# Optimization experiments

Hardware: AMD Instinct MI355X
Metric: run time of the kernel (lower is better)

Reference implementation:

```python
import jax, jax.numpy as jnp
import numpy as np

B, N, D, H, S = 64, 1000, 512, 8, 20
DK = D // H
TANH_CLIP = 10.0
NEG = -1e9


def setup_inputs() -> dict:
    key = jax.random.key(0)
    k1, k2, k3, k4, k5 = jax.random.split(key, 5)
    embeddings = jax.random.normal(k1, (B, N, D), dtype=jnp.float32)
    q = jax.random.normal(k2, (B, S, D), dtype=jnp.float32)
    # action_mask: True = feasible. Ensure at least one feasible node per row.
    action_mask = jax.random.bernoulli(k3, 0.5, (B, S, N))
    action_mask = action_mask.at[:, :, 0].set(True)
    W_kvl = jax.random.normal(k4, (D, 3 * D), dtype=jnp.float32) * (1.0 / np.sqrt(D))
    W_out = jax.random.normal(k5, (D, D), dtype=jnp.float32) * (1.0 / np.sqrt(D))
    return {"embeddings": embeddings, "q": q, "action_mask": action_mask,
            "W_kvl": W_kvl, "W_out": W_out}


def reference(embeddings, q, action_mask, W_kvl, W_out):
    # _precompute: project node embeddings into glimpse K, V and logit K
    kvl = jnp.einsum('bnd,de->bne', embeddings, W_kvl)  # [B,N,3D]
    glimpse_k, glimpse_v, logit_k = jnp.split(kvl, 3, axis=-1)
    # dynamic embedding is zero (StaticEmbedding for TSP)

    mask = ~action_mask  # True = infeasible, shape [B,S,N]

    # multi-head glimpse attention
    qh = q.reshape(B, S, H, DK)
    kh = glimpse_k.reshape(B, N, H, DK)
    vh = glimpse_v.reshape(B, N, H, DK)
    compat = jnp.einsum('bshd,bnhd->bhsn', qh, kh) / np.sqrt(DK)
    compat = jnp.where(mask[:, None, :, :], NEG, compat)
    attn = jax.nn.softmax(compat, axis=-1)
    heads = jnp.einsum('bhsn,bnhd->bshd', attn, vh).reshape(B, S, D)
    glimpse = jnp.einsum('bsd,de->bse', heads, W_out)  # [B,S,D]

    # pointer logits against logit_k, tanh clipping, mask, log-softmax
    logits = jnp.einsum('bsd,bnd->bsn', glimpse, logit_k) / np.sqrt(D)
    logits = TANH_CLIP * jnp.tanh(logits)
    logits = jnp.where(mask, NEG, logits)
    log_p = jax.nn.log_softmax(logits, axis=-1)  # [B,S,N]

    # rearrange 'b s l -> (s b) l'
    return jnp.swapaxes(log_p, 0, 1).reshape(S * B, N)
```

## Files before the change

### kernel.cpp

```cpp
#include <hip/hip_runtime.h>

#define BB 64
#define NN 1000
#define NP 1024
#define DD 512
#define HH 8
#define SS 20
#define NEGV -1e9f

typedef float v4f __attribute__((ext_vector_type(4)));
typedef short v8s __attribute__((ext_vector_type(8)));
typedef int   v8i __attribute__((ext_vector_type(8)));
typedef int   v4i __attribute__((ext_vector_type(4)));
typedef unsigned char uchar;
typedef unsigned long long ulong_t;

static __device__ __forceinline__ short f2bf(float f) {
    unsigned u = __builtin_bit_cast(unsigned, f);
    u = (u + 0x7fffu + ((u >> 16) & 1u)) >> 16;
    return (short)u;
}
static __device__ __forceinline__ float bf2f(short s) {
    unsigned u = ((unsigned)(unsigned short)s) << 16;
    return __builtin_bit_cast(float, u);
}
static __device__ __forceinline__ uchar f2fp8(float f) {
    return (uchar)(__builtin_amdgcn_cvt_pk_fp8_f32(f, 0.f, 0, false) & 0xff);
}

static __device__ __forceinline__ void gld16(const void* g, void* l) {
    __builtin_amdgcn_global_load_lds(
        (const __attribute__((address_space(1))) void*)(g),
        (__attribute__((address_space(3))) void*)(l),
        16, 0, 0);
}

__global__ void prep(const float* __restrict__ Wkvl, uchar* __restrict__ Wt8,
                     const float* __restrict__ Wout, short* __restrict__ Wot,
                     const float* __restrict__ emb, int* __restrict__ emb8) {
    __shared__ float t[32][33];
    int bid = blockIdx.x, tid = threadIdx.x;
    if (bid < 768) {
        int c0 = (bid % 48) * 32, r0 = (bid / 48) * 32;
        int x = tid & 31, y = tid >> 5;
        for (int k = 0; k < 32; k += 8)
            t[y + k][x] = Wkvl[(long)(r0 + y + k) * 1536 + c0 + x];
        __syncthreads();
        for (int k = 0; k < 32; k += 8)
            Wt8[(long)(c0 + y + k) * 512 + r0 + x] = f2fp8(t[x][y + k]);
    } else if (bid < 1024) {
        int bb = bid - 768;
        int c0 = (bb & 15) * 32, r0 = (bb >> 4) * 32;
        int x = tid & 31, y = tid >> 5;
        for (int k = 0; k < 32; k += 8)
            t[y + k][x] = Wout[(long)(r0 + y + k) * 512 + c0 + x];
        __syncthreads();
        for (int k = 0; k < 32; k += 8)
            Wot[(long)(c0 + y + k) * 512 + r0 + x] = f2bf(t[x][y + k]);
    } else {
        int i = (bid - 1024) * 256 + tid;
        long o = (long)i * 8;
        v4f a = *(const v4f*)(emb + o);
        v4f b = *(const v4f*)(emb + o + 4);
        int lo = __builtin_amdgcn_cvt_pk_fp8_f32(a.x, a.y, 0, false);
        lo = __builtin_amdgcn_cvt_pk_fp8_f32(a.z, a.w, lo, true);
        int hi = __builtin_amdgcn_cvt_pk_fp8_f32(b.x, b.y, 0, false);
        hi = __builtin_amdgcn_cvt_pk_fp8_f32(b.z, b.w, hi, true);
        int2 r; r.x = lo; r.y = hi;
        *(int2*)(emb8 + i * 2) = r;
    }
}

__global__ __launch_bounds__(256) void gemm_kvl(const uchar* __restrict__ emb8,
                                                const uchar* __restrict__ Wt8,
                                                uchar* __restrict__ kvl8) {
    extern __shared__ __align__(16) uchar smem[];
    uchar* As0 = smem;
    uchar* Bs0 = smem + 32768;
    int tid = threadIdx.x;
    int id = blockIdx.x;
    int wgid = (id & 7) * 750 + (id >> 3);
    int m_idx = wgid / 12, n_idx = wgid - m_idx * 12;
    int m0 = m_idx * 128, n0 = n_idx * 128;
    int wid = tid >> 6, lane = tid & 63, quad = lane >> 4, l16 = lane & 15;
    int wm = wid & 1, wn = wid >> 1;
    const uchar* Ag = emb8 + (long)m0 * 512;
    const uchar* Bg = Wt8 + (long)n0 * 512;
    int rsub = lane >> 3;
    int kc = ((lane & 7) ^ rsub) * 16;

    v4f acc[4][4] = {};

    auto stageAB = [&](int bi, int kk) {
        #pragma unroll
        for (int p = 0; p < 4; ++p) {
            int rl = wid * 32 + p * 8;
            gld16(Ag + (long)(rl + rsub) * 512 + kk + kc, As0 + bi * 16384 + rl * 128);
        }
        #pragma unroll
        for (int p = 0; p < 4; ++p) {
            int rl = wid * 32 + p * 8;
            gld16(Bg + (long)(rl + rsub) * 512 + kk + kc, Bs0 + bi * 16384 + rl * 128);
        }
    };
    auto ldfrag = [&](const uchar* base, int row) -> v8i {
        int c0 = (quad * 2) ^ (row & 7);
        v4i lo = *(const v4i*)(base + row * 128 + c0 * 16);
        v4i hi = *(const v4i*)(base + row * 128 + (c0 ^ 1) * 16);
        return __builtin_shufflevector(lo, hi, 0, 1, 2, 3, 4, 5, 6, 7);
    };

    stageAB(0, 0);
    stageAB(1, 128);
    asm volatile("s_waitcnt vmcnt(8)" ::: "memory");
    __builtin_amdgcn_s_barrier();
    __builtin_amdgcn_sched_barrier(0);

    v8i af[4], bf[4];
    #pragma unroll
    for (int t = 0; t < 4; ++t) {
        int cur = t & 1;
        const uchar* ab = As0 + cur * 16384;
        const uchar* bb = Bs0 + cur * 16384;
        #pragma unroll
        for (int i = 0; i < 4; ++i) af[i] = ldfrag(ab, wm * 64 + i * 16 + l16);
        #pragma unroll
        for (int j = 0; j < 4; ++j) bf[j] = ldfrag(bb, wn * 64 + j * 16 + l16);
        __builtin_amdgcn_s_setprio(1);
        #pragma unroll
        for (int i = 0; i < 4; ++i)
            #pragma unroll
            for (int j = 0; j < 2; ++j)
                acc[i][j] = __builtin_amdgcn_mfma_scale_f32_16x16x128_f8f6f4(
                    af[i], bf[j], acc[i][j], 0, 0, 0, 0x7f7f7f7f, 0, 0x7f7f7f7f);
        __builtin_amdgcn_s_setprio(0);
        asm volatile("s_waitcnt lgkmcnt(0)" ::: "memory");
        __builtin_amdgcn_s_barrier();
        if (t < 2) stageAB(cur, (t + 2) * 128);
        __builtin_amdgcn_s_setprio(1);
        #pragma unroll
        for (int i = 0; i < 4; ++i)
            #pragma unroll
            for (int j = 2; j < 4; ++j)
                acc[i][j] = __builtin_amdgcn_mfma_scale_f32_16x16x128_f8f6f4(
                    af[i], bf[j], acc[i][j], 0, 0, 0, 0x7f7f7f7f, 0, 0x7f7f7f7f);
        __builtin_amdgcn_s_setprio(0);
        if (t < 3) {
            if (t < 2) asm volatile("s_waitcnt vmcnt(8)" ::: "memory");
            else       asm volatile("s_waitcnt vmcnt(0)" ::: "memory");
            __builtin_amdgcn_s_barrier();
            __builtin_amdgcn_sched_barrier(0);
        }
    }
    __syncthreads();

    short* rp = (short*)smem;
    short* r = rp + wid * (16 * 72);
    #pragma unroll
    for (int i = 0; i < 4; ++i) {
        #pragma unroll
        for (int jj = 0; jj < 4; ++jj)
            #pragma unroll
            for (int rr = 0; rr < 4; ++rr)
                r[(quad * 4 + rr) * 72 + jj * 16 + l16] = f2bf(acc[i][jj][rr]);
        #pragma unroll
        for (int h = 0; h < 2; ++h) {
            int rowl = h * 8 + (lane >> 3);
            int colc = (lane & 7) * 8;
            v8s val = *(const v8s*)(r + rowl * 72 + colc);
            int lo = __builtin_amdgcn_cvt_pk_fp8_f32(bf2f(val[0]), bf2f(val[1]), 0, false);
            lo = __builtin_amdgcn_cvt_pk_fp8_f32(bf2f(val[2]), bf2f(val[3]), lo, true);
            int hi = __builtin_amdgcn_cvt_pk_fp8_f32(bf2f(val[4]), bf2f(val[5]), 0, false);
            hi = __builtin_amdgcn_cvt_pk_fp8_f32(bf2f(val[6]), bf2f(val[7]), hi, true);
            int2 st; st.x = lo; st.y = hi;
            *(int2*)(kvl8 + (long)(m0 + wm * 64 + i * 16 + rowl) * 1536 +
                     n0 + wn * 64 + colc) = st;
        }
    }
}

__global__ void pack_kv(const uchar* __restrict__ kvl8, uchar* __restrict__ Kf,
                        uchar* __restrict__ Vf) {
    int bh = blockIdx.x, b = bh >> 3, h = bh & 7;
    int g = blockIdx.y;
    __shared__ uchar Kl[64][72];
    __shared__ uchar VT[64][72];
    int tid = threadIdx.x;
    int node_l = tid >> 2, chunk = (tid & 3) * 16;
    int gn = g * 64 + node_l;
    int ncl = gn < NN ? gn : NN - 1;
    const uchar* rowp = kvl8 + ((long)b * NN + ncl) * 1536 + h * 64;
    *(v4i*)&Kl[node_l][chunk] = *(const v4i*)(rowp + chunk);
    {
        const uchar* vp = rowp + 512 + chunk;
        ulong_t v0 = *(const ulong_t*)(vp);
        ulong_t v1 = *(const ulong_t*)(vp + 8);
        uchar* b0p = (uchar*)&v0; uchar* b1p = (uchar*)&v1;
        #pragma unroll
        for (int j = 0; j < 8; ++j) VT[chunk + j][node_l] = b0p[j];
        #pragma unroll
        for (int j = 0; j < 8; ++j) VT[chunk + 8 + j][node_l] = b1p[j];
    }
    __syncthreads();
    int wid = tid >> 6, lane = tid & 63, l16 = lane & 15, quad = lane >> 4;
    #pragma unroll
    for (int ks = 0; ks < 2; ++ks) {
        ulong_t frag = *(const ulong_t*)&Kl[wid * 16 + l16][ks * 32 + quad * 8];
        *(ulong_t*)(Kf + (((long)bh * 64 + g * 4 + wid) * 2 + ks) * 512 + lane * 8) = frag;
    }
    #pragma unroll
    for (int sub = 0; sub < 2; ++sub) {
        ulong_t frag = *(const ulong_t*)&VT[wid * 16 + l16][sub * 32 + quad * 8];
        *(ulong_t*)(Vf + (((long)bh * 4 + wid) * 32 + g * 2 + sub) * 512 + lane * 8) = frag;
    }
}

#define CST 1036
__global__ __launch_bounds__(512) void attn_fused(const float* __restrict__ q,
                                                  const uchar* __restrict__ Kf,
                                                  const uchar* __restrict__ Vf,
                                                  const int* __restrict__ mask,
                                                  float* __restrict__ heads) {
    int b = blockIdx.x, h = blockIdx.y;
    __shared__ __align__(16) uchar qs[32 * 72];
    __shared__ __align__(16) short cmp[SS * CST];
    int tid = threadIdx.x, wid = tid >> 6, lane = tid & 63, quad = lane >> 4, l16 = lane & 15;
    for (int i = tid; i < 32 * 64; i += 512) {
        int row = i >> 6, col = i & 63;
        float v = (row < SS) ? q[((long)b * SS + row) * DD + h * 64 + col] : 0.f;
        qs[row * 72 + col] = f2fp8(v);
    }
    __syncthreads();
    long af[2][2];
    #pragma unroll
    for (int mt = 0; mt < 2; ++mt)
        #pragma unroll
        for (int ks = 0; ks < 2; ++ks)
            af[mt][ks] = *(const long*)(qs + (mt * 16 + l16) * 72 + ks * 32 + quad * 8);
    const uchar* kfb = Kf + ((long)(b * HH + h) * 64) * 1024;
    for (int t = 0; t < 8; ++t) {
        int nt = wid * 8 + t;
        long b0 = *(const long*)(kfb + (long)nt * 1024 + lane * 8);
        long b1 = *(const long*)(kfb + (long)nt * 1024 + 512 + lane * 8);
        #pragma unroll
        for (int mt = 0; mt < 2; ++mt) {
            v4f a = {};
            a = __builtin_amdgcn_mfma_f32_16x16x32_fp8_fp8(af[mt][0], b0, a, 0, 0, 0);
            a = __builtin_amdgcn_mfma_f32_16x16x32_fp8_fp8(af[mt][1], b1, a, 0, 0, 0);
            #pragma unroll
            for (int r = 0; r < 4; ++r) {
                int s = mt * 16 + quad * 4 + r;
                if (s < SS) cmp[s * CST + nt * 16 + l16] = f2bf(a[r] * 0.125f);
            }
        }
    }
    __syncthreads();
    for (int s = wid; s < SS; s += 8) {
        const int* mr = mask + ((long)b * SS + s) * NN;
        float x[16];
        float mx = NEGV;
        #pragma unroll
        for (int i = 0; i < 16; ++i) {
            int n = lane + 64 * i;
            float v = bf2f(cmp[s * CST + n]);
            bool feas = (n < NN) && (mr[n < NN ? n : 0] != 0);
            x[i] = feas ? v : NEGV;
            mx = fmaxf(mx, x[i]);
        }
        for (int off = 32; off; off >>= 1) mx = fmaxf(mx, __shfl_xor(mx, off));
        float sum = 0.f;
        #pragma unroll
        for (int i = 0; i < 16; ++i) { x[i] = __expf(x[i] - mx); sum += x[i]; }
        for (int off = 32; off; off >>= 1) sum += __shfl_xor(sum, off);
        float inv = 1.0f / sum;
        uchar* pr = (uchar*)cmp + (long)s * (CST * 2);
        #pragma unroll
        for (int i = 0; i < 16; ++i) pr[lane + 64 * i] = f2fp8(x[i] * inv);
    }
    __syncthreads();
    int mt = wid & 1, dt = wid >> 1;
    int srow = mt * 16 + l16; if (srow > SS - 1) srow = SS - 1;
    const uchar* ap = (const uchar*)cmp + (long)srow * (CST * 2) + quad * 8;
    const uchar* vfb = Vf + (((long)(b * HH + h) * 4 + dt) * 32) * 512;
    v4f acc = {};
    for (int k0s = 0; k0s < 32; ++k0s) {
        long afr = *(const long*)(ap + k0s * 32);
        long bfr = *(const long*)(vfb + (long)k0s * 512 + lane * 8);
        acc = __builtin_amdgcn_mfma_f32_16x16x32_fp8_fp8(afr, bfr, acc, 0, 0, 0);
    }
    #pragma unroll
    for (int r = 0; r < 4; ++r) {
        int s = mt * 16 + quad * 4 + r;
        if (s < SS)
            heads[((long)b * SS + s) * DD + h * 64 + dt * 16 + l16] = acc[r];
    }
}

__global__ __launch_bounds__(256) void out_proj(const float* __restrict__ heads,
                                                const short* __restrict__ Wot,
                                                float* __restrict__ glimpse) {
    __shared__ __align__(16) short As[64 * 40], Bs[64 * 40];
    int tid = threadIdx.x;
    int m0 = blockIdx.x * 64, n0 = blockIdx.y * 64;
    int wid = tid >> 6, lane = tid & 63, quad = lane >> 4, l16 = lane & 15;
    int wm = wid & 1, wn = wid >> 1;
    int arow = tid >> 3, akol = (tid & 7) * 4;
    int brow = tid >> 2, bkol = (tid & 3) * 8;
    v4f acc[2][2] = {};
    for (int kk = 0; kk < 512; kk += 32) {
        #pragma unroll
        for (int p = 0; p < 2; ++p) {
            int r = arow + p * 32;
            v4f a = *(const v4f*)(heads + (long)(m0 + r) * 512 + kk + akol);
            short4 s4;
            s4.x = f2bf(a.x); s4.y = f2bf(a.y); s4.z = f2bf(a.z); s4.w = f2bf(a.w);
            *(short4*)(As + r * 40 + akol) = s4;
        }
        *(uint4*)(Bs + brow * 40 + bkol) =
            *(const uint4*)(Wot + (long)(n0 + brow) * 512 + kk + bkol);
        __syncthreads();
        #pragma unroll
        for (int i = 0; i < 2; ++i) {
            v8s af = *(const v8s*)(As + (wm * 32 + i * 16 + l16) * 40 + quad * 8);
            #pragma unroll
            for (int j = 0; j < 2; ++j) {
                v8s bf = *(const v8s*)(Bs + (wn * 32 + j * 16 + l16) * 40 + quad * 8);
                acc[i][j] = __builtin_amdgcn_mfma_f32_16x16x32_bf16(af, bf, acc[i][j], 0, 0, 0);
            }
        }
        __syncthreads();
    }
    #pragma unroll
    for (int i = 0; i < 2; ++i)
        #pragma unroll
        for (int j = 0; j < 2; ++j)
            #pragma unroll
            for (int r = 0; r < 4; ++r)
                glimpse[(long)(m0 + wm * 32 + i * 16 + quad * 4 + r) * 512 +
                        n0 + wn * 32 + j * 16 + l16] = acc[i][j][r];
}

__global__ __launch_bounds__(256) void ptr_logits(const float* __restrict__ glimpse,
                                                  const uchar* __restrict__ kvl8,
                                                  float* __restrict__ logits) {
    int b = blockIdx.x, g = blockIdx.y;
    __shared__ __align__(16) uchar Gs[32 * 520];
    int tid = threadIdx.x;
    #pragma unroll
    for (int it = 0; it < 16; ++it) {
        int e = it * 1024 + tid * 4;
        int row = e >> 9, col = e & 511;
        int pk = 0;
        if (row < SS) {
            v4f a = *(const v4f*)(glimpse + ((long)b * SS + row) * 512 + col);
            pk = __builtin_amdgcn_cvt_pk_fp8_f32(a.x, a.y, 0, false);
            pk = __builtin_amdgcn_cvt_pk_fp8_f32(a.z, a.w, pk, true);
        }
        *(int*)(Gs + row * 520 + col) = pk;
    }
    __syncthreads();
    int wid = tid >> 6, lane = tid & 63, quad = lane >> 4, l16 = lane & 15;
    const float scale = 0.04419417382415922f;
    int nt = g * 4 + wid;
    int n = nt * 16 + l16;
    int ncl = n < NN ? n : NN - 1;
    const uchar* kp = kvl8 + ((long)b * NN + ncl) * 1536 + 1024 + quad * 8;
    v4f acc[2] = {};
    for (int k = 0; k < 16; ++k) {
        long bfr = *(const long*)(kp + k * 32);
        #pragma unroll
        for (int m = 0; m < 2; ++m) {
            long afr = *(const long*)(Gs + (m * 16 + l16) * 520 + k * 32 + quad * 8);
            acc[m] = __builtin_amdgcn_mfma_f32_16x16x32_fp8_fp8(afr, bfr, acc[m], 0, 0, 0);
        }
    }
    #pragma unroll
    for (int m = 0; m < 2; ++m)
        #pragma unroll
        for (int r = 0; r < 4; ++r) {
            int s = m * 16 + quad * 4 + r;
            if (s < SS)
                logits[((long)b * SS + s) * NP + nt * 16 + l16] = acc[m][r] * scale;
        }
}

__global__ __launch_bounds__(256) void logsoftmax_out(const float* __restrict__ logits,
                                                      const int* __restrict__ mask,
                                                      float* __restrict__ out) {
    int row = blockIdx.x;
    int b = row / SS, s = row % SS;
    int tid = threadIdx.x;
    __shared__ float red[8];
    int n0 = tid * 4;
    v4f v = *(const v4f*)(logits + (long)row * NP + n0);
    const int* mr = mask + (long)row * NN;
    float x[4];
    float mx = NEGV;
    #pragma unroll
    for (int j = 0; j < 4; ++j) {
        int n = n0 + j;
        float t = 10.f * tanhf(v[j]);
        bool feas = (n < NN) && (mr[n < NN ? n : 0] != 0);
        x[j] = feas ? t : NEGV;
        mx = fmaxf(mx, x[j]);
    }
    for (int off = 32; off; off >>= 1) mx = fmaxf(mx, __shfl_xor(mx, off));
    int wid = tid >> 6, lane = tid & 63;
    if (lane == 0) red[wid] = mx;
    __syncthreads();
    mx = fmaxf(fmaxf(red[0], red[1]), fmaxf(red[2], red[3]));
    float sum = 0.f;
    #pragma unroll
    for (int j = 0; j < 4; ++j) sum += __expf(x[j] - mx);
    for (int off = 32; off; off >>= 1) sum += __shfl_xor(sum, off);
    __syncthreads();
    if (lane == 0) red[4 + wid] = sum;
    __syncthreads();
    sum = red[4] + red[5] + red[6] + red[7];
    float lse = mx + __logf(sum);
    float* orow = out + ((long)s * BB + b) * NN;
    #pragma unroll
    for (int j = 0; j < 4; ++j) {
        int n = n0 + j;
        if (n < NN) orow[n] = x[j] - lse;
    }
}

extern "C" void kernel_launch(void* const* d_in, const int* in_sizes, int n_in,
                              void* d_out, int out_size, void* d_ws, size_t ws_size,
                              hipStream_t stream) {
    const float* emb  = (const float*)d_in[0];
    const float* q    = (const float*)d_in[1];
    const int*   mask = (const int*)d_in[2];
    const float* Wkvl = (const float*)d_in[3];
    const float* Wout = (const float*)d_in[4];
    float* out = (float*)d_out;

    char* ws = (char*)d_ws;
    uchar* kvl8    = (uchar*)ws; ws += (size_t)64000 * 1536;
    uchar* Vt8     = (uchar*)ws; ws += (size_t)512 * 64 * NP;
    uchar* Wt8     = (uchar*)ws; ws += (size_t)1536 * 512;
    uchar* emb8    = (uchar*)ws; ws += (size_t)64000 * 512;
    short* Wot     = (short*)ws; ws += (size_t)512 * 512 * 2;
    float* heads   = (float*)ws; ws += (size_t)BB * SS * DD * 4;
    float* glimpse = (float*)ws; ws += (size_t)BB * SS * DD * 4;
    float* logits  = (float*)ws; ws += (size_t)BB * SS * NP * 4;

    uchar* Kf = Wt8;
    uchar* Vf = Vt8;

    static int s_attr_done = 0;
    if (!s_attr_done) {
        hipFuncSetAttribute(reinterpret_cast<const void*>(gemm_kvl),
                            hipFuncAttributeMaxDynamicSharedMemorySize, 65536);
        s_attr_done = 1;
    }

    prep<<<dim3(1024 + 16000), 256, 0, stream>>>(Wkvl, Wt8, Wout, Wot, emb, (int*)emb8);
    gemm_kvl<<<dim3(6000), 256, 65536, stream>>>(emb8, Wt8, kvl8);
    pack_kv<<<dim3(512, 16), 256, 0, stream>>>(kvl8, Kf, Vf);
    attn_fused<<<dim3(BB, HH), 512, 0, stream>>>(q, Kf, Vf, mask, heads);
    out_proj<<<dim3(20, 8), 256, 0, stream>>>(heads, Wot, glimpse);
    ptr_logits<<<dim3(BB, 16), 256, 0, stream>>>(glimpse, kvl8, logits);
    logsoftmax_out<<<dim3(BB * SS), 256, 0, stream>>>(logits, mask, out);
}
```

Measured before the change: 349.2 us.

## Fuse K/V fragment packing into GEMM epilogue and drop pack_kv kernel

The projection GEMM's epilogue now writes glimpse K and V straight into the MFMA-fragment layouts (Kf, and a transposed Vf) used by the attention kernel. The logit K goes to its own compact buffer with a 512-byte row stride. This removes the separate pack_kv launch and the round trip of the full 1536-wide fp8 kvl tensor through memory. The V epilogue does scattered 8-byte stores with transposition from shared memory and explicitly zeroes the padding past the last node. The attention PV loop also splits its accumulation across four independent accumulators to break the MFMA dependency chain.

```diff
diff --git a/kernel.cpp b/kernel.cpp
--- a/kernel.cpp
+++ b/kernel.cpp
@@ -73,7 +73,9 @@
 
 __global__ __launch_bounds__(256) void gemm_kvl(const uchar* __restrict__ emb8,
                                                 const uchar* __restrict__ Wt8,
-                                                uchar* __restrict__ kvl8) {
+                                                uchar* __restrict__ Kf,
+                                                uchar* __restrict__ Vf,
+                                                uchar* __restrict__ kvlL) {
     extern __shared__ __align__(16) uchar smem[];
     uchar* As0 = smem;
     uchar* Bs0 = smem + 32768;
@@ -156,6 +158,7 @@
 
     short* rp = (short*)smem;
     short* r = rp + wid * (16 * 72);
+    int nw = n0 + wn * 64;
     #pragma unroll
     for (int i = 0; i < 4; ++i) {
         #pragma unroll
@@ -163,55 +166,71 @@
             #pragma unroll
             for (int rr = 0; rr < 4; ++rr)
                 r[(quad * 4 + rr) * 72 + jj * 16 + l16] = f2bf(acc[i][jj][rr]);
-        #pragma unroll
-        for (int h = 0; h < 2; ++h) {
-            int rowl = h * 8 + (lane >> 3);
-            int colc = (lane & 7) * 8;
-            v8s val = *(const v8s*)(r + rowl * 72 + colc);
-            int lo = __builtin_amdgcn_cvt_pk_fp8_f32(bf2f(val[0]), bf2f(val[1]), 0, false);
-            lo = __builtin_amdgcn_cvt_pk_fp8_f32(bf2f(val[2]), bf2f(val[3]), lo, true);
-            int hi = __builtin_amdgcn_cvt_pk_fp8_f32(bf2f(val[4]), bf2f(val[5]), 0, false);
-            hi = __builtin_amdgcn_cvt_pk_fp8_f32(bf2f(val[6]), bf2f(val[7]), hi, true);
-            int2 st; st.x = lo; st.y = hi;
-            *(int2*)(kvl8 + (long)(m0 + wm * 64 + i * 16 + rowl) * 1536 +
-                     n0 + wn * 64 + colc) = st;
-        }
-    }
-}
-
-__global__ void pack_kv(const uchar* __restrict__ kvl8, uchar* __restrict__ Kf,
-                        uchar* __restrict__ Vf) {
-    int bh = blockIdx.x, b = bh >> 3, h = bh & 7;
-    int g = blockIdx.y;
-    __shared__ uchar Kl[64][72];
-    __shared__ uchar VT[64][72];
-    int tid = threadIdx.x;
-    int node_l = tid >> 2, chunk = (tid & 3) * 16;
-    int gn = g * 64 + node_l;
-    int ncl = gn < NN ? gn : NN - 1;
-    const uchar* rowp = kvl8 + ((long)b * NN + ncl) * 1536 + h * 64;
-    *(v4i*)&Kl[node_l][chunk] = *(const v4i*)(rowp + chunk);
-    {
-        const uchar* vp = rowp + 512 + chunk;
-        ulong_t v0 = *(const ulong_t*)(vp);
-        ulong_t v1 = *(const ulong_t*)(vp + 8);
-        uchar* b0p = (uchar*)&v0; uchar* b1p = (uchar*)&v1;
-        #pragma unroll
-        for (int j = 0; j < 8; ++j) VT[chunk + j][node_l] = b0p[j];
-        #pragma unroll
-        for (int j = 0; j < 8; ++j) VT[chunk + 8 + j][node_l] = b1p[j];
-    }
-    __syncthreads();
-    int wid = tid >> 6, lane = tid & 63, l16 = lane & 15, quad = lane >> 4;
-    #pragma unroll
-    for (int ks = 0; ks < 2; ++ks) {
-        ulong_t frag = *(const ulong_t*)&Kl[wid * 16 + l16][ks * 32 + quad * 8];
-        *(ulong_t*)(Kf + (((long)bh * 64 + g * 4 + wid) * 2 + ks) * 512 + lane * 8) = frag;
-    }
-    #pragma unroll
-    for (int sub = 0; sub < 2; ++sub) {
-        ulong_t frag = *(const ulong_t*)&VT[wid * 16 + l16][sub * 32 + quad * 8];
-        *(ulong_t*)(Vf + (((long)bh * 4 + wid) * 32 + g * 2 + sub) * 512 + lane * 8) = frag;
+        int sub0 = m0 + wm * 64 + i * 16;
+        if (n_idx < 4) {
+            int hK = nw >> 6;
+            #pragma unroll
+            for (int h2 = 0; h2 < 2; ++h2) {
+                int rowl = h2 * 8 + (lane >> 3);
+                int colc = (lane & 7) * 8;
+                v8s val = *(const v8s*)(r + rowl * 72 + colc);
+                int lo = __builtin_amdgcn_cvt_pk_fp8_f32(bf2f(val[0]), bf2f(val[1]), 0, false);
+                lo = __builtin_amdgcn_cvt_pk_fp8_f32(bf2f(val[2]), bf2f(val[3]), lo, true);
+                int hi = __builtin_amdgcn_cvt_pk_fp8_f32(bf2f(val[4]), bf2f(val[5]), 0, false);
+                hi = __builtin_amdgcn_cvt_pk_fp8_f32(bf2f(val[6]), bf2f(val[7]), hi, true);
+                int node = sub0 + rowl;
+                int b = node / 1000, nl = node - b * 1000;
+                long addr = (((long)(b * 8 + hK) * 64 + (nl >> 4)) * 2 + (colc >> 5)) * 512
+                            + ((((colc & 31) >> 3) * 16 + (nl & 15)) * 8);
+                int2 st; st.x = lo; st.y = hi;
+                *(int2*)(Kf + addr) = st;
+            }
+        } else if (n_idx < 8) {
+            int hV = (nw - 512) >> 6;
+            int o = lane >> 5, dl = lane & 31;
+            int node0 = sub0 + o * 8;
+            int b = node0 / 1000, nl = node0 - b * 1000;
+            int bh4 = (b * 8 + hV) * 4;
+            int quadv = (nl & 31) >> 3;
+            #pragma unroll
+            for (int u = 0; u < 2; ++u) {
+                int d = u * 32 + dl;
+                float f0 = bf2f(r[(o * 8 + 0) * 72 + d]);
+                float f1 = bf2f(r[(o * 8 + 1) * 72 + d]);
+                float f2 = bf2f(r[(o * 8 + 2) * 72 + d]);
+                float f3 = bf2f(r[(o * 8 + 3) * 72 + d]);
+                float f4 = bf2f(r[(o * 8 + 4) * 72 + d]);
+                float f5 = bf2f(r[(o * 8 + 5) * 72 + d]);
+                float f6 = bf2f(r[(o * 8 + 6) * 72 + d]);
+                float f7 = bf2f(r[(o * 8 + 7) * 72 + d]);
+                int lo = __builtin_amdgcn_cvt_pk_fp8_f32(f0, f1, 0, false);
+                lo = __builtin_amdgcn_cvt_pk_fp8_f32(f2, f3, lo, true);
+                int hi = __builtin_amdgcn_cvt_pk_fp8_f32(f4, f5, 0, false);
+                hi = __builtin_amdgcn_cvt_pk_fp8_f32(f6, f7, hi, true);
+                long base = ((long)(bh4 + (d >> 4)) * 32 + (nl >> 5)) * 512 + (d & 15) * 8;
+                int2 st; st.x = lo; st.y = hi;
+                *(int2*)(Vf + base + quadv * 128) = st;
+                if (nl == 992) {
+                    int2 z; z.x = 0; z.y = 0;
+                    *(int2*)(Vf + base + 1 * 128) = z;
+                    *(int2*)(Vf + base + 2 * 128) = z;
+                    *(int2*)(Vf + base + 3 * 128) = z;
+                }
+            }
+        } else {
+            #pragma unroll
+            for (int h2 = 0; h2 < 2; ++h2) {
+                int rowl = h2 * 8 + (lane >> 3);
+                int colc = (lane & 7) * 8;
+                v8s val = *(const v8s*)(r + rowl * 72 + colc);
+                int lo = __builtin_amdgcn_cvt_pk_fp8_f32(bf2f(val[0]), bf2f(val[1]), 0, false);
+                lo = __builtin_amdgcn_cvt_pk_fp8_f32(bf2f(val[2]), bf2f(val[3]), lo, true);
+                int hi = __builtin_amdgcn_cvt_pk_fp8_f32(bf2f(val[4]), bf2f(val[5]), 0, false);
+                hi = __builtin_amdgcn_cvt_pk_fp8_f32(bf2f(val[6]), bf2f(val[7]), hi, true);
+                int2 st; st.x = lo; st.y = hi;
+                *(int2*)(kvlL + (long)(sub0 + rowl) * 512 + (nw - 1024) + colc) = st;
+            }
+        }
     }
 }
 
@@ -282,17 +301,27 @@
     int srow = mt * 16 + l16; if (srow > SS - 1) srow = SS - 1;
     const uchar* ap = (const uchar*)cmp + (long)srow * (CST * 2) + quad * 8;
     const uchar* vfb = Vf + (((long)(b * HH + h) * 4 + dt) * 32) * 512;
-    v4f acc = {};
-    for (int k0s = 0; k0s < 32; ++k0s) {
-        long afr = *(const long*)(ap + k0s * 32);
-        long bfr = *(const long*)(vfb + (long)k0s * 512 + lane * 8);
-        acc = __builtin_amdgcn_mfma_f32_16x16x32_fp8_fp8(afr, bfr, acc, 0, 0, 0);
-    }
+    v4f a0 = {}, a1 = {}, a2 = {}, a3 = {};
+    for (int k0s = 0; k0s < 32; k0s += 4) {
+        a0 = __builtin_amdgcn_mfma_f32_16x16x32_fp8_fp8(
+            *(const long*)(ap + k0s * 32),
+            *(const long*)(vfb + (long)k0s * 512 + lane * 8), a0, 0, 0, 0);
+        a1 = __builtin_amdgcn_mfma_f32_16x16x32_fp8_fp8(
+            *(const long*)(ap + (k0s + 1) * 32),
+            *(const long*)(vfb + (long)(k0s + 1) * 512 + lane * 8), a1, 0, 0, 0);
+        a2 = __builtin_amdgcn_mfma_f32_16x16x32_fp8_fp8(
+            *(const long*)(ap + (k0s + 2) * 32),
+            *(const long*)(vfb + (long)(k0s + 2) * 512 + lane * 8), a2, 0, 0, 0);
+        a3 = __builtin_amdgcn_mfma_f32_16x16x32_fp8_fp8(
+            *(const long*)(ap + (k0s + 3) * 32),
+            *(const long*)(vfb + (long)(k0s + 3) * 512 + lane * 8), a3, 0, 0, 0);
+    }
+    v4f accv = (a0 + a1) + (a2 + a3);
     #pragma unroll
     for (int r = 0; r < 4; ++r) {
         int s = mt * 16 + quad * 4 + r;
         if (s < SS)
-            heads[((long)b * SS + s) * DD + h * 64 + dt * 16 + l16] = acc[r];
+            heads[((long)b * SS + s) * DD + h * 64 + dt * 16 + l16] = accv[r];
     }
 }
 
@@ -341,7 +370,7 @@
 }
 
 __global__ __launch_bounds__(256) void ptr_logits(const float* __restrict__ glimpse,
-                                                  const uchar* __restrict__ kvl8,
+                                                  const uchar* __restrict__ kvlL,
                                                   float* __restrict__ logits) {
     int b = blockIdx.x, g = blockIdx.y;
     __shared__ __align__(16) uchar Gs[32 * 520];
@@ -364,7 +393,7 @@
     int nt = g * 4 + wid;
     int n = nt * 16 + l16;
     int ncl = n < NN ? n : NN - 1;
-    const uchar* kp = kvl8 + ((long)b * NN + ncl) * 1536 + 1024 + quad * 8;
+    const uchar* kp = kvlL + ((long)b * NN + ncl) * 512 + quad * 8;
     v4f acc[2] = {};
     for (int k = 0; k < 16; ++k) {
         long bfr = *(const long*)(kp + k * 32);
@@ -437,8 +466,9 @@
     float* out = (float*)d_out;
 
     char* ws = (char*)d_ws;
-    uchar* kvl8    = (uchar*)ws; ws += (size_t)64000 * 1536;
-    uchar* Vt8     = (uchar*)ws; ws += (size_t)512 * 64 * NP;
+    uchar* kvlL    = (uchar*)ws; ws += (size_t)64000 * 512;
+    uchar* Vf      = (uchar*)ws; ws += (size_t)512 * 64 * 1024;
+    uchar* Kf      = (uchar*)ws; ws += (size_t)512 * 64 * 1024;
     uchar* Wt8     = (uchar*)ws; ws += (size_t)1536 * 512;
     uchar* emb8    = (uchar*)ws; ws += (size_t)64000 * 512;
     short* Wot     = (short*)ws; ws += (size_t)512 * 512 * 2;
@@ -446,9 +476,6 @@
     float* glimpse = (float*)ws; ws += (size_t)BB * SS * DD * 4;
     float* logits  = (float*)ws; ws += (size_t)BB * SS * NP * 4;
 
-    uchar* Kf = Wt8;
-    uchar* Vf = Vt8;
-
     static int s_attr_done = 0;
     if (!s_attr_done) {
         hipFuncSetAttribute(reinterpret_cast<const void*>(gemm_kvl),
@@ -457,10 +484,9 @@
     }
 
     prep<<<dim3(1024 + 16000), 256, 0, stream>>>(Wkvl, Wt8, Wout, Wot, emb, (int*)emb8);
-    gemm_kvl<<<dim3(6000), 256, 65536, stream>>>(emb8, Wt8, kvl8);
-    pack_kv<<<dim3(512, 16), 256, 0, stream>>>(kvl8, Kf, Vf);
+    gemm_kvl<<<dim3(6000), 256, 65536, stream>>>(emb8, Wt8, Kf, Vf, kvlL);
     attn_fused<<<dim3(BB, HH), 512, 0, stream>>>(q, Kf, Vf, mask, heads);
     out_proj<<<dim3(20, 8), 256, 0, stream>>>(heads, Wot, glimpse);
-    ptr_logits<<<dim3(BB, 16), 256, 0, stream>>>(glimpse, kvl8, logits);
+    ptr_logits<<<dim3(BB, 16), 256, 0, stream>>>(glimpse, kvlL, logits);
     logsoftmax_out<<<dim3(BB * SS), 256, 0, stream>>>(logits, mask, out);
 }
```

Measured after the change: 361.7 us. +3.6%, slower.

## Fuse output projection, pointer logits and log-softmax into one per-batch kernel

Applied to the files above, without the earlier changes.

Replaces the out_proj, ptr_logits and logsoftmax_out kernels with a single head_out kernel. It runs one 512-thread block per batch element and keeps glimpse and logits in shared memory instead of round-tripping through global memory. The attention PV loop now splits into four independent accumulators to shorten the MFMA dependency chain. The cost is that only 64 blocks run, each with about 130KB of LDS, so parallelism is much lower than the previous grids. Glimpse is also rounded to bf16 before the fp8 conversion, which adds a small extra rounding step.

```diff
diff --git a/kernel.cpp b/kernel.cpp
--- a/kernel.cpp
+++ b/kernel.cpp
@@ -282,147 +282,137 @@
     int srow = mt * 16 + l16; if (srow > SS - 1) srow = SS - 1;
     const uchar* ap = (const uchar*)cmp + (long)srow * (CST * 2) + quad * 8;
     const uchar* vfb = Vf + (((long)(b * HH + h) * 4 + dt) * 32) * 512;
-    v4f acc = {};
-    for (int k0s = 0; k0s < 32; ++k0s) {
-        long afr = *(const long*)(ap + k0s * 32);
-        long bfr = *(const long*)(vfb + (long)k0s * 512 + lane * 8);
-        acc = __builtin_amdgcn_mfma_f32_16x16x32_fp8_fp8(afr, bfr, acc, 0, 0, 0);
-    }
+    v4f a0 = {}, a1 = {}, a2 = {}, a3 = {};
+    for (int k0s = 0; k0s < 32; k0s += 4) {
+        a0 = __builtin_amdgcn_mfma_f32_16x16x32_fp8_fp8(
+            *(const long*)(ap + k0s * 32),
+            *(const long*)(vfb + (long)k0s * 512 + lane * 8), a0, 0, 0, 0);
+        a1 = __builtin_amdgcn_mfma_f32_16x16x32_fp8_fp8(
+            *(const long*)(ap + (k0s + 1) * 32),
+            *(const long*)(vfb + (long)(k0s + 1) * 512 + lane * 8), a1, 0, 0, 0);
+        a2 = __builtin_amdgcn_mfma_f32_16x16x32_fp8_fp8(
+            *(const long*)(ap + (k0s + 2) * 32),
+            *(const long*)(vfb + (long)(k0s + 2) * 512 + lane * 8), a2, 0, 0, 0);
+        a3 = __builtin_amdgcn_mfma_f32_16x16x32_fp8_fp8(
+            *(const long*)(ap + (k0s + 3) * 32),
+            *(const long*)(vfb + (long)(k0s + 3) * 512 + lane * 8), a3, 0, 0, 0);
+    }
+    v4f accv = (a0 + a1) + (a2 + a3);
     #pragma unroll
     for (int r = 0; r < 4; ++r) {
         int s = mt * 16 + quad * 4 + r;
         if (s < SS)
-            heads[((long)b * SS + s) * DD + h * 64 + dt * 16 + l16] = acc[r];
-    }
-}
-
-__global__ __launch_bounds__(256) void out_proj(const float* __restrict__ heads,
+            heads[((long)b * SS + s) * DD + h * 64 + dt * 16 + l16] = accv[r];
+    }
+}
+
+__global__ __launch_bounds__(512) void head_out(const float* __restrict__ heads,
                                                 const short* __restrict__ Wot,
-                                                float* __restrict__ glimpse) {
-    __shared__ __align__(16) short As[64 * 40], Bs[64 * 40];
-    int tid = threadIdx.x;
-    int m0 = blockIdx.x * 64, n0 = blockIdx.y * 64;
-    int wid = tid >> 6, lane = tid & 63, quad = lane >> 4, l16 = lane & 15;
-    int wm = wid & 1, wn = wid >> 1;
-    int arow = tid >> 3, akol = (tid & 7) * 4;
-    int brow = tid >> 2, bkol = (tid & 3) * 8;
-    v4f acc[2][2] = {};
+                                                const uchar* __restrict__ kvl8,
+                                                const int* __restrict__ mask,
+                                                float* __restrict__ out) {
+    extern __shared__ __align__(16) uchar hsm[];
+    short* As = (short*)hsm;
+    uchar* Gs = hsm + 33280;
+    float* Lg = (float*)(hsm + 33280 + 16640);
+    int b = blockIdx.x;
+    int tid = threadIdx.x, wid = tid >> 6, lane = tid & 63, quad = lane >> 4, l16 = lane & 15;
+
+    for (int u = tid; u < 32 * 128; u += 512) {
+        int row = u >> 7, c4 = (u & 127) * 4;
+        short4 s4;
+        if (row < SS) {
+            v4f a = *(const v4f*)(heads + ((long)b * SS + row) * 512 + c4);
+            s4.x = f2bf(a.x); s4.y = f2bf(a.y); s4.z = f2bf(a.z); s4.w = f2bf(a.w);
+        } else { s4.x = 0; s4.y = 0; s4.z = 0; s4.w = 0; }
+        *(short4*)(As + row * 520 + c4) = s4;
+    }
+    __syncthreads();
+
+    int n0w = wid * 64;
+    v4f acc[2][4] = {};
     for (int kk = 0; kk < 512; kk += 32) {
-        #pragma unroll
-        for (int p = 0; p < 2; ++p) {
-            int r = arow + p * 32;
-            v4f a = *(const v4f*)(heads + (long)(m0 + r) * 512 + kk + akol);
-            short4 s4;
-            s4.x = f2bf(a.x); s4.y = f2bf(a.y); s4.z = f2bf(a.z); s4.w = f2bf(a.w);
-            *(short4*)(As + r * 40 + akol) = s4;
-        }
-        *(uint4*)(Bs + brow * 40 + bkol) =
-            *(const uint4*)(Wot + (long)(n0 + brow) * 512 + kk + bkol);
-        __syncthreads();
-        #pragma unroll
-        for (int i = 0; i < 2; ++i) {
-            v8s af = *(const v8s*)(As + (wm * 32 + i * 16 + l16) * 40 + quad * 8);
-            #pragma unroll
-            for (int j = 0; j < 2; ++j) {
-                v8s bf = *(const v8s*)(Bs + (wn * 32 + j * 16 + l16) * 40 + quad * 8);
-                acc[i][j] = __builtin_amdgcn_mfma_f32_16x16x32_bf16(af, bf, acc[i][j], 0, 0, 0);
+        v8s afr[2], bfr[4];
+        #pragma unroll
+        for (int m = 0; m < 2; ++m)
+            afr[m] = *(const v8s*)(As + (m * 16 + l16) * 520 + kk + quad * 8);
+        #pragma unroll
+        for (int j = 0; j < 4; ++j)
+            bfr[j] = *(const v8s*)(Wot + (long)(n0w + j * 16 + l16) * 512 + kk + quad * 8);
+        #pragma unroll
+        for (int m = 0; m < 2; ++m)
+            #pragma unroll
+            for (int j = 0; j < 4; ++j)
+                acc[m][j] = __builtin_amdgcn_mfma_f32_16x16x32_bf16(afr[m], bfr[j], acc[m][j], 0, 0, 0);
+    }
+    __syncthreads();
+    #pragma unroll
+    for (int m = 0; m < 2; ++m)
+        #pragma unroll
+        for (int j = 0; j < 4; ++j)
+            #pragma unroll
+            for (int r = 0; r < 4; ++r)
+                As[(m * 16 + quad * 4 + r) * 520 + n0w + j * 16 + l16] = f2bf(acc[m][j][r]);
+    __syncthreads();
+
+    for (int u = tid; u < 32 * 128; u += 512) {
+        int row = u >> 7, c4 = (u & 127) * 4;
+        short4 s4 = *(const short4*)(As + row * 520 + c4);
+        int pk = __builtin_amdgcn_cvt_pk_fp8_f32(bf2f(s4.x), bf2f(s4.y), 0, false);
+        pk = __builtin_amdgcn_cvt_pk_fp8_f32(bf2f(s4.z), bf2f(s4.w), pk, true);
+        *(int*)(Gs + row * 520 + c4) = pk;
+    }
+    __syncthreads();
+
+    const float scale = 0.04419417382415922f;
+    for (int g = 0; g < 8; ++g) {
+        int nt = wid * 8 + g;
+        int n = nt * 16 + l16;
+        int ncl = n < NN ? n : NN - 1;
+        const uchar* kp = kvl8 + ((long)b * NN + ncl) * 1536 + 1024 + quad * 8;
+        v4f acc2[2] = {};
+        for (int k = 0; k < 16; ++k) {
+            long bfr = *(const long*)(kp + k * 32);
+            #pragma unroll
+            for (int m = 0; m < 2; ++m) {
+                long afr2 = *(const long*)(Gs + (m * 16 + l16) * 520 + k * 32 + quad * 8);
+                acc2[m] = __builtin_amdgcn_mfma_f32_16x16x32_fp8_fp8(afr2, bfr, acc2[m], 0, 0, 0);
             }
         }
-        __syncthreads();
-    }
-    #pragma unroll
-    for (int i = 0; i < 2; ++i)
-        #pragma unroll
-        for (int j = 0; j < 2; ++j)
-            #pragma unroll
-            for (int r = 0; r < 4; ++r)
-                glimpse[(long)(m0 + wm * 32 + i * 16 + quad * 4 + r) * 512 +
-                        n0 + wn * 32 + j * 16 + l16] = acc[i][j][r];
-}
-
-__global__ __launch_bounds__(256) void ptr_logits(const float* __restrict__ glimpse,
-                                                  const uchar* __restrict__ kvl8,
-                                                  float* __restrict__ logits) {
-    int b = blockIdx.x, g = blockIdx.y;
-    __shared__ __align__(16) uchar Gs[32 * 520];
-    int tid = threadIdx.x;
-    #pragma unroll
-    for (int it = 0; it < 16; ++it) {
-        int e = it * 1024 + tid * 4;
-        int row = e >> 9, col = e & 511;
-        int pk = 0;
-        if (row < SS) {
-            v4f a = *(const v4f*)(glimpse + ((long)b * SS + row) * 512 + col);
-            pk = __builtin_amdgcn_cvt_pk_fp8_f32(a.x, a.y, 0, false);
-            pk = __builtin_amdgcn_cvt_pk_fp8_f32(a.z, a.w, pk, true);
-        }
-        *(int*)(Gs + row * 520 + col) = pk;
-    }
-    __syncthreads();
-    int wid = tid >> 6, lane = tid & 63, quad = lane >> 4, l16 = lane & 15;
-    const float scale = 0.04419417382415922f;
-    int nt = g * 4 + wid;
-    int n = nt * 16 + l16;
-    int ncl = n < NN ? n : NN - 1;
-    const uchar* kp = kvl8 + ((long)b * NN + ncl) * 1536 + 1024 + quad * 8;
-    v4f acc[2] = {};
-    for (int k = 0; k < 16; ++k) {
-        long bfr = *(const long*)(kp + k * 32);
-        #pragma unroll
-        for (int m = 0; m < 2; ++m) {
-            long afr = *(const long*)(Gs + (m * 16 + l16) * 520 + k * 32 + quad * 8);
-            acc[m] = __builtin_amdgcn_mfma_f32_16x16x32_fp8_fp8(afr, bfr, acc[m], 0, 0, 0);
-        }
-    }
-    #pragma unroll
-    for (int m = 0; m < 2; ++m)
-        #pragma unroll
-        for (int r = 0; r < 4; ++r) {
-            int s = m * 16 + quad * 4 + r;
-            if (s < SS)
-                logits[((long)b * SS + s) * NP + nt * 16 + l16] = acc[m][r] * scale;
-        }
-}
-
-__global__ __launch_bounds__(256) void logsoftmax_out(const float* __restrict__ logits,
-                                                      const int* __restrict__ mask,
-                                                      float* __restrict__ out) {
-    int row = blockIdx.x;
-    int b = row / SS, s = row % SS;
-    int tid = threadIdx.x;
-    __shared__ float red[8];
-    int n0 = tid * 4;
-    v4f v = *(const v4f*)(logits + (long)row * NP + n0);
-    const int* mr = mask + (long)row * NN;
-    float x[4];
-    float mx = NEGV;
-    #pragma unroll
-    for (int j = 0; j < 4; ++j) {
-        int n = n0 + j;
-        float t = 10.f * tanhf(v[j]);
-        bool feas = (n < NN) && (mr[n < NN ? n : 0] != 0);
-        x[j] = feas ? t : NEGV;
-        mx = fmaxf(mx, x[j]);
-    }
-    for (int off = 32; off; off >>= 1) mx = fmaxf(mx, __shfl_xor(mx, off));
-    int wid = tid >> 6, lane = tid & 63;
-    if (lane == 0) red[wid] = mx;
-    __syncthreads();
-    mx = fmaxf(fmaxf(red[0], red[1]), fmaxf(red[2], red[3]));
-    float sum = 0.f;
-    #pragma unroll
-    for (int j = 0; j < 4; ++j) sum += __expf(x[j] - mx);
-    for (int off = 32; off; off >>= 1) sum += __shfl_xor(sum, off);
-    __syncthreads();
-    if (lane == 0) red[4 + wid] = sum;
-    __syncthreads();
-    sum = red[4] + red[5] + red[6] + red[7];
-    float lse = mx + __logf(sum);
-    float* orow = out + ((long)s * BB + b) * NN;
-    #pragma unroll
-    for (int j = 0; j < 4; ++j) {
-        int n = n0 + j;
-        if (n < NN) orow[n] = x[j] - lse;
+        #pragma unroll
+        for (int m = 0; m < 2; ++m)
+            #pragma unroll
+            for (int r = 0; r < 4; ++r) {
+                int s = m * 16 + quad * 4 + r;
+                if (s < SS) Lg[s * 1040 + nt * 16 + l16] = acc2[m][r] * scale;
+            }
+    }
+    __syncthreads();
+
+    for (int s = wid; s < SS; s += 8) {
+        const int* mr = mask + ((long)b * SS + s) * NN;
+        float x[16];
+        float mx = NEGV;
+        #pragma unroll
+        for (int i = 0; i < 16; ++i) {
+            int n = lane + 64 * i;
+            float t = 10.f * tanhf(Lg[s * 1040 + n]);
+            bool feas = (n < NN) && (mr[n < NN ? n : 0] != 0);
+            x[i] = feas ? t : NEGV;
+            mx = fmaxf(mx, x[i]);
+        }
+        for (int off = 32; off; off >>= 1) mx = fmaxf(mx, __shfl_xor(mx, off));
+        float sum = 0.f;
+        #pragma unroll
+        for (int i = 0; i < 16; ++i) sum += __expf(x[i] - mx);
+        for (int off = 32; off; off >>= 1) sum += __shfl_xor(sum, off);
+        float lse = mx + __logf(sum);
+        float* orow = out + ((long)s * BB + b) * NN;
+        #pragma unroll
+        for (int i = 0; i < 16; ++i) {
+            int n = lane + 64 * i;
+            if (n < NN) orow[n] = x[i] - lse;
+        }
     }
 }
 
@@ -438,21 +428,20 @@
 
     char* ws = (char*)d_ws;
     uchar* kvl8    = (uchar*)ws; ws += (size_t)64000 * 1536;
-    uchar* Vt8     = (uchar*)ws; ws += (size_t)512 * 64 * NP;
+    uchar* Vf      = (uchar*)ws; ws += (size_t)512 * 64 * NP;
     uchar* Wt8     = (uchar*)ws; ws += (size_t)1536 * 512;
     uchar* emb8    = (uchar*)ws; ws += (size_t)64000 * 512;
     short* Wot     = (short*)ws; ws += (size_t)512 * 512 * 2;
     float* heads   = (float*)ws; ws += (size_t)BB * SS * DD * 4;
-    float* glimpse = (float*)ws; ws += (size_t)BB * SS * DD * 4;
-    float* logits  = (float*)ws; ws += (size_t)BB * SS * NP * 4;
 
     uchar* Kf = Wt8;
-    uchar* Vf = Vt8;
 
     static int s_attr_done = 0;
     if (!s_attr_done) {
         hipFuncSetAttribute(reinterpret_cast<const void*>(gemm_kvl),
                             hipFuncAttributeMaxDynamicSharedMemorySize, 65536);
+        hipFuncSetAttribute(reinterpret_cast<const void*>(head_out),
+                            hipFuncAttributeMaxDynamicSharedMemorySize, 133120);
         s_attr_done = 1;
     }
 
@@ -460,7 +449,5 @@
     gemm_kvl<<<dim3(6000), 256, 65536, stream>>>(emb8, Wt8, kvl8);
     pack_kv<<<dim3(512, 16), 256, 0, stream>>>(kvl8, Kf, Vf);
     attn_fused<<<dim3(BB, HH), 512, 0, stream>>>(q, Kf, Vf, mask, heads);
-    out_proj<<<dim3(20, 8), 256, 0, stream>>>(heads, Wot, glimpse);
-    ptr_logits<<<dim3(BB, 16), 256, 0, stream>>>(glimpse, kvl8, logits);
-    logsoftmax_out<<<dim3(BB * SS), 256, 0, stream>>>(logits, mask, out);
-}
+    head_out<<<dim3(BB), 512, 133120, stream>>>(heads, Wot, kvl8, mask, out);
+}
```

Result: slower. 374.2 us (+7.2%).

## Split KVL GEMM tile across eight waves and unroll attention PV accumulators

Applied to the files above, without the earlier changes.

The projection GEMM now launches 512 threads per 128x128 tile. Each of eight waves computes a 64x32 sub-tile, so per-thread accumulators, staging loads and the epilogue shrink. This aims to raise wave-level parallelism and hide latency better, at the cost of more waves sharing LDS bandwidth and barriers. Separately, the attention PV loop uses four independent MFMA accumulators to break the serial dependency chain, summing them at the end.

```diff
diff --git a/kernel.cpp b/kernel.cpp
--- a/kernel.cpp
+++ b/kernel.cpp
@@ -71,7 +71,7 @@
     }
 }
 
-__global__ __launch_bounds__(256) void gemm_kvl(const uchar* __restrict__ emb8,
+__global__ __launch_bounds__(512) void gemm_kvl(const uchar* __restrict__ emb8,
                                                 const uchar* __restrict__ Wt8,
                                                 uchar* __restrict__ kvl8) {
     extern __shared__ __align__(16) uchar smem[];
@@ -89,17 +89,17 @@
     int rsub = lane >> 3;
     int kc = ((lane & 7) ^ rsub) * 16;
 
-    v4f acc[4][4] = {};
+    v4f acc[4][2] = {};
 
     auto stageAB = [&](int bi, int kk) {
         #pragma unroll
-        for (int p = 0; p < 4; ++p) {
-            int rl = wid * 32 + p * 8;
+        for (int p = 0; p < 2; ++p) {
+            int rl = wid * 16 + p * 8;
             gld16(Ag + (long)(rl + rsub) * 512 + kk + kc, As0 + bi * 16384 + rl * 128);
         }
         #pragma unroll
-        for (int p = 0; p < 4; ++p) {
-            int rl = wid * 32 + p * 8;
+        for (int p = 0; p < 2; ++p) {
+            int rl = wid * 16 + p * 8;
             gld16(Bg + (long)(rl + rsub) * 512 + kk + kc, Bs0 + bi * 16384 + rl * 128);
         }
     };
@@ -112,11 +112,11 @@
 
     stageAB(0, 0);
     stageAB(1, 128);
-    asm volatile("s_waitcnt vmcnt(8)" ::: "memory");
+    asm volatile("s_waitcnt vmcnt(4)" ::: "memory");
     __builtin_amdgcn_s_barrier();
     __builtin_amdgcn_sched_barrier(0);
 
-    v8i af[4], bf[4];
+    v8i af[4], bf[2];
     #pragma unroll
     for (int t = 0; t < 4; ++t) {
         int cur = t & 1;
@@ -125,14 +125,12 @@
         #pragma unroll
         for (int i = 0; i < 4; ++i) af[i] = ldfrag(ab, wm * 64 + i * 16 + l16);
         #pragma unroll
-        for (int j = 0; j < 4; ++j) bf[j] = ldfrag(bb, wn * 64 + j * 16 + l16);
+        for (int j = 0; j < 2; ++j) bf[j] = ldfrag(bb, wn * 32 + j * 16 + l16);
         __builtin_amdgcn_s_setprio(1);
         #pragma unroll
         for (int i = 0; i < 4; ++i)
-            #pragma unroll
-            for (int j = 0; j < 2; ++j)
-                acc[i][j] = __builtin_amdgcn_mfma_scale_f32_16x16x128_f8f6f4(
-                    af[i], bf[j], acc[i][j], 0, 0, 0, 0x7f7f7f7f, 0, 0x7f7f7f7f);
+            acc[i][0] = __builtin_amdgcn_mfma_scale_f32_16x16x128_f8f6f4(
+                af[i], bf[0], acc[i][0], 0, 0, 0, 0x7f7f7f7f, 0, 0x7f7f7f7f);
         __builtin_amdgcn_s_setprio(0);
         asm volatile("s_waitcnt lgkmcnt(0)" ::: "memory");
         __builtin_amdgcn_s_barrier();
@@ -140,13 +138,11 @@
         __builtin_amdgcn_s_setprio(1);
         #pragma unroll
         for (int i = 0; i < 4; ++i)
-            #pragma unroll
-            for (int j = 2; j < 4; ++j)
-                acc[i][j] = __builtin_amdgcn_mfma_scale_f32_16x16x128_f8f6f4(
-                    af[i], bf[j], acc[i][j], 0, 0, 0, 0x7f7f7f7f, 0, 0x7f7f7f7f);
+            acc[i][1] = __builtin_amdgcn_mfma_scale_f32_16x16x128_f8f6f4(
+                af[i], bf[1], acc[i][1], 0, 0, 0, 0x7f7f7f7f, 0, 0x7f7f7f7f);
         __builtin_amdgcn_s_setprio(0);
         if (t < 3) {
-            if (t < 2) asm volatile("s_waitcnt vmcnt(8)" ::: "memory");
+            if (t < 2) asm volatile("s_waitcnt vmcnt(4)" ::: "memory");
             else       asm volatile("s_waitcnt vmcnt(0)" ::: "memory");
             __builtin_amdgcn_s_barrier();
             __builtin_amdgcn_sched_barrier(0);
@@ -155,26 +151,26 @@
     __syncthreads();
 
     short* rp = (short*)smem;
-    short* r = rp + wid * (16 * 72);
+    short* r = rp + wid * (16 * 40);
+    int nw = n0 + wn * 32;
     #pragma unroll
     for (int i = 0; i < 4; ++i) {
         #pragma unroll
-        for (int jj = 0; jj < 4; ++jj)
+        for (int jj = 0; jj < 2; ++jj)
             #pragma unroll
             for (int rr = 0; rr < 4; ++rr)
-                r[(quad * 4 + rr) * 72 + jj * 16 + l16] = f2bf(acc[i][jj][rr]);
-        #pragma unroll
-        for (int h = 0; h < 2; ++h) {
-            int rowl = h * 8 + (lane >> 3);
-            int colc = (lane & 7) * 8;
-            v8s val = *(const v8s*)(r + rowl * 72 + colc);
+                r[(quad * 4 + rr) * 40 + jj * 16 + l16] = f2bf(acc[i][jj][rr]);
+        {
+            int rowl = lane >> 2;
+            int colc = (lane & 3) * 8;
+            v8s val = *(const v8s*)(r + rowl * 40 + colc);
             int lo = __builtin_amdgcn_cvt_pk_fp8_f32(bf2f(val[0]), bf2f(val[1]), 0, false);
             lo = __builtin_amdgcn_cvt_pk_fp8_f32(bf2f(val[2]), bf2f(val[3]), lo, true);
             int hi = __builtin_amdgcn_cvt_pk_fp8_f32(bf2f(val[4]), bf2f(val[5]), 0, false);
             hi = __builtin_amdgcn_cvt_pk_fp8_f32(bf2f(val[6]), bf2f(val[7]), hi, true);
             int2 st; st.x = lo; st.y = hi;
             *(int2*)(kvl8 + (long)(m0 + wm * 64 + i * 16 + rowl) * 1536 +
-                     n0 + wn * 64 + colc) = st;
+                     nw + colc) = st;
         }
     }
 }
@@ -282,17 +278,27 @@
     int srow = mt * 16 + l16; if (srow > SS - 1) srow = SS - 1;
     const uchar* ap = (const uchar*)cmp + (long)srow * (CST * 2) + quad * 8;
     const uchar* vfb = Vf + (((long)(b * HH + h) * 4 + dt) * 32) * 512;
-    v4f acc = {};
-    for (int k0s = 0; k0s < 32; ++k0s) {
-        long afr = *(const long*)(ap + k0s * 32);
-        long bfr = *(const long*)(vfb + (long)k0s * 512 + lane * 8);
-        acc = __builtin_amdgcn_mfma_f32_16x16x32_fp8_fp8(afr, bfr, acc, 0, 0, 0);
-    }
+    v4f a0 = {}, a1 = {}, a2 = {}, a3 = {};
+    for (int k0s = 0; k0s < 32; k0s += 4) {
+        a0 = __builtin_amdgcn_mfma_f32_16x16x32_fp8_fp8(
+            *(const long*)(ap + k0s * 32),
+            *(const long*)(vfb + (long)k0s * 512 + lane * 8), a0, 0, 0, 0);
+        a1 = __builtin_amdgcn_mfma_f32_16x16x32_fp8_fp8(
+            *(const long*)(ap + (k0s + 1) * 32),
+            *(const long*)(vfb + (long)(k0s + 1) * 512 + lane * 8), a1, 0, 0, 0);
+        a2 = __builtin_amdgcn_mfma_f32_16x16x32_fp8_fp8(
+            *(const long*)(ap + (k0s + 2) * 32),
+            *(const long*)(vfb + (long)(k0s + 2) * 512 + lane * 8), a2, 0, 0, 0);
+        a3 = __builtin_amdgcn_mfma_f32_16x16x32_fp8_fp8(
+            *(const long*)(ap + (k0s + 3) * 32),
+            *(const long*)(vfb + (long)(k0s + 3) * 512 + lane * 8), a3, 0, 0, 0);
+    }
+    v4f accv = (a0 + a1) + (a2 + a3);
     #pragma unroll
     for (int r = 0; r < 4; ++r) {
         int s = mt * 16 + quad * 4 + r;
         if (s < SS)
-            heads[((long)b * SS + s) * DD + h * 64 + dt * 16 + l16] = acc[r];
+            heads[((long)b * SS + s) * DD + h * 64 + dt * 16 + l16] = accv[r];
     }
 }
 
@@ -438,7 +444,7 @@
 
     char* ws = (char*)d_ws;
     uchar* kvl8    = (uchar*)ws; ws += (size_t)64000 * 1536;
-    uchar* Vt8     = (uchar*)ws; ws += (size_t)512 * 64 * NP;
+    uchar* Vf      = (uchar*)ws; ws += (size_t)512 * 64 * NP;
     uchar* Wt8     = (uchar*)ws; ws += (size_t)1536 * 512;
     uchar* emb8    = (uchar*)ws; ws += (size_t)64000 * 512;
     short* Wot     = (short*)ws; ws += (size_t)512 * 512 * 2;
@@ -447,7 +453,6 @@
     float* logits  = (float*)ws; ws += (size_t)BB * SS * NP * 4;
 
     uchar* Kf = Wt8;
-    uchar* Vf = Vt8;
 
     static int s_attr_done = 0;
     if (!s_attr_done) {
@@ -457,7 +462,7 @@
     }
 
     prep<<<dim3(1024 + 16000), 256, 0, stream>>>(Wkvl, Wt8, Wout, Wot, emb, (int*)emb8);
-    gemm_kvl<<<dim3(6000), 256, 65536, stream>>>(emb8, Wt8, kvl8);
+    gemm_kvl<<<dim3(6000), 512, 65536, stream>>>(emb8, Wt8, kvl8);
     pack_kv<<<dim3(512, 16), 256, 0, stream>>>(kvl8, Kf, Vf);
     attn_fused<<<dim3(BB, HH), 512, 0, stream>>>(q, Kf, Vf, mask, heads);
     out_proj<<<dim3(20, 8), 256, 0, stream>>>(heads, Wot, glimpse);
```

Result: no change. 347.3 us (-0.6%).
